# Optimization experiments

Measured on AMD Instinct MI355X. Metric: run time of the kernel, lower is better.

## Reference

```python
import jax, jax.numpy as jnp
import numpy as np

B, N, DIM, H, DH = 4, 2048, 512, 8, 64
INNER = H * DH  # 512
SCALE = DH ** -0.5


def setup_inputs() -> dict:
    key = jax.random.key(0)
    k1, k2, k3, k4 = jax.random.split(key, 4)
    x = jax.random.normal(k1, (B, N, DIM), dtype=jnp.float32)
    bias = jax.random.normal(k2, (B, N, DIM), dtype=jnp.float32)
    # to_qkv: Linear(dim, inner*3, bias=False)
    w_qkv = jax.random.normal(k3, (DIM, 3 * INNER), dtype=jnp.float32) * (DIM ** -0.5)
    # to_out: Linear(inner, dim) with bias (project_out=True since heads != 1)
    w_out = jax.random.normal(k4, (INNER, DIM), dtype=jnp.float32) * (INNER ** -0.5)
    b_out = jnp.zeros((DIM,), dtype=jnp.float32)
    return {"x": x, "bias": bias, "w_qkv": w_qkv, "w_out": w_out, "b_out": b_out}


def _split_heads(t):
    # [b, n, h*d] -> [b, h, n, d]
    b, n, _ = t.shape
    return t.reshape(b, n, H, DH).transpose(0, 2, 1, 3)


def reference(x, bias, w_qkv, w_out, b_out):
    qkv = x @ w_qkv  # [b, n, 3*inner]
    q, k, v = jnp.split(qkv, 3, axis=-1)
    q, k, v = map(_split_heads, (q, k, v))
    dots = jnp.einsum('bhid,bhjd->bhij', q, k) * SCALE  # [b,h,n,n]

    qkv_b = bias @ w_qkv
    qb, kb, _ = jnp.split(qkv_b, 3, axis=-1)
    qb, kb = _split_heads(qb), _split_heads(kb)
    dots = dots + jnp.einsum('bhid,bhjd->bhij', qb, kb) * SCALE

    attn = jax.nn.softmax(dots, axis=-1)
    out = jnp.einsum('bhij,bhjd->bhid', attn, v)  # [b,h,n,d]
    out = out.transpose(0, 2, 1, 3).reshape(x.shape[0], x.shape[1], INNER)
    return out @ w_out + b_out
```

## Files before the change

kernel.cpp:

```cpp
#include <hip/hip_runtime.h>
#include <hip/hip_bf16.h>

#define DEV __device__ __forceinline__

typedef __attribute__((ext_vector_type(8))) short short8;
typedef __attribute__((ext_vector_type(4))) short sv4;
typedef __attribute__((ext_vector_type(4))) float f32x4;

constexpr int B = 4, N = 2048, DIM = 512, H = 8, DH = 64;
constexpr int INNER = H * DH;
constexpr int BH = B * H;
constexpr float SCALE = 0.125f;

constexpr size_t OFF_WQKVT = 0;
constexpr size_t OFF_WOUTT = OFF_WQKVT + (size_t)1536 * 512;
constexpr size_t OFF_QT    = OFF_WOUTT + (size_t)512 * 512;
constexpr size_t OFF_KT    = OFF_QT + (size_t)BH * N * 128;
constexpr size_t OFF_VT    = OFF_KT + (size_t)BH * N * 128;
constexpr size_t OFF_AO    = OFF_VT + (size_t)BH * DH * N;

DEV short f2b(float f) {
    __hip_bfloat16 h = __float2bfloat16(f);
    return __builtin_bit_cast(short, h);
}

DEV void gload16(const void* g, void* l) {
    __builtin_amdgcn_global_load_lds(
        (const __attribute__((address_space(1))) unsigned int*)g,
        (__attribute__((address_space(3))) unsigned int*)l, 16, 0, 0);
}

__global__ void prep_kernel(const float* __restrict__ wqkv,
                            const float* __restrict__ wout,
                            __hip_bfloat16* __restrict__ ws) {
    __hip_bfloat16* wqkvT = ws + OFF_WQKVT;
    __hip_bfloat16* woutT = ws + OFF_WOUTT;
    int tid = blockIdx.x * blockDim.x + threadIdx.x;
    const int total1 = 512 * 1536 / 4;
    const int total2 = 512 * 512 / 4;
    for (int i = tid; i < total1 + total2; i += gridDim.x * blockDim.x) {
        if (i < total1) {
            int k  = i / 384;
            int c4 = (i % 384) * 4;
            float4 v = ((const float4*)wqkv)[i];
            wqkvT[(size_t)(c4 + 0) * 512 + k] = __float2bfloat16(v.x);
            wqkvT[(size_t)(c4 + 1) * 512 + k] = __float2bfloat16(v.y);
            wqkvT[(size_t)(c4 + 2) * 512 + k] = __float2bfloat16(v.z);
            wqkvT[(size_t)(c4 + 3) * 512 + k] = __float2bfloat16(v.w);
        } else {
            int j  = i - total1;
            int k  = j / 128;
            int c4 = (j % 128) * 4;
            float4 v = ((const float4*)wout)[j];
            woutT[(size_t)(c4 + 0) * 512 + k] = __float2bfloat16(v.x);
            woutT[(size_t)(c4 + 1) * 512 + k] = __float2bfloat16(v.y);
            woutT[(size_t)(c4 + 2) * 512 + k] = __float2bfloat16(v.z);
            woutT[(size_t)(c4 + 3) * 512 + k] = __float2bfloat16(v.w);
        }
    }
}

__global__ __launch_bounds__(256) void gemm_qkv(const float* __restrict__ x,
                                                const float* __restrict__ bias,
                                                __hip_bfloat16* __restrict__ ws) {
    int mt = blockIdx.x, yt = blockIdx.y;
    bool src_is_bias = (yt >= 12);
    int nt = src_is_bias ? yt - 12 : yt;
    const float* A = src_is_bias ? bias : x;
    const __hip_bfloat16* Bt = ws + OFF_WQKVT;
    int m0 = mt * 128, n0 = nt * 128;

    __shared__ __align__(16) short As[128][72];
    __shared__ __align__(16) short Bs[128][72];

    int tid  = threadIdx.x;
    int wave = tid >> 6, lane = tid & 63;
    int wrow = wave >> 1, wcol = wave & 1;
    int lg = lane >> 4, li = lane & 15;

    f32x4 acc[4][4] = {};

    for (int k0 = 0; k0 < 512; k0 += 64) {
#pragma unroll
        for (int r = 0; r < 4; ++r) {
            int idx = (tid + r * 256) * 8;
            int row = idx >> 6, kk = idx & 63;
            const float* srcA = A + (size_t)(m0 + row) * 512 + k0 + kk;
            float4 v0 = ((const float4*)srcA)[0];
            float4 v1 = ((const float4*)srcA)[1];
            short8 sv;
            sv[0] = f2b(v0.x); sv[1] = f2b(v0.y); sv[2] = f2b(v0.z); sv[3] = f2b(v0.w);
            sv[4] = f2b(v1.x); sv[5] = f2b(v1.y); sv[6] = f2b(v1.z); sv[7] = f2b(v1.w);
            *(short8*)(&As[row][kk]) = sv;
            const __hip_bfloat16* srcB = Bt + (size_t)(n0 + row) * 512 + k0 + kk;
            *(short8*)(&Bs[row][kk]) = *(const short8*)srcB;
        }
        __syncthreads();
#pragma unroll
        for (int ks = 0; ks < 2; ++ks) {
            short8 af[4], bf[4];
#pragma unroll
            for (int m = 0; m < 4; ++m)
                af[m] = *(const short8*)(&As[wrow * 64 + m * 16 + li][ks * 32 + lg * 8]);
#pragma unroll
            for (int n = 0; n < 4; ++n)
                bf[n] = *(const short8*)(&Bs[wcol * 64 + n * 16 + li][ks * 32 + lg * 8]);
#pragma unroll
            for (int m = 0; m < 4; ++m)
#pragma unroll
                for (int n = 0; n < 4; ++n)
                    acc[m][n] = __builtin_amdgcn_mfma_f32_16x16x32_bf16(af[m], bf[n], acc[m][n], 0, 0, 0);
        }
        __syncthreads();
    }

    __hip_bfloat16* QT = ws + OFF_QT;
    __hip_bfloat16* KT = ws + OFF_KT;
    __hip_bfloat16* VT = ws + OFF_VT;
    int qkoff = src_is_bias ? 64 : 0;
#pragma unroll
    for (int m = 0; m < 4; ++m)
#pragma unroll
        for (int n = 0; n < 4; ++n)
#pragma unroll
            for (int j = 0; j < 4; ++j) {
                int row = m0 + wrow * 64 + m * 16 + lg * 4 + j;
                int col = n0 + wcol * 64 + n * 16 + li;
                float v = acc[m][n][j];
                int b = row >> 11, nn = row & 2047;
                if (col < 512) {
                    int h = col >> 6, d = col & 63;
                    QT[((size_t)(b * H + h) * N + nn) * 128 + d + qkoff] = __float2bfloat16(v * SCALE);
                } else if (col < 1024) {
                    int c = col - 512; int h = c >> 6, d = c & 63;
                    KT[((size_t)(b * H + h) * N + nn) * 128 + d + qkoff] = __float2bfloat16(v);
                } else {
                    int c = col - 1024; int h = c >> 6, d = c & 63;
                    VT[((size_t)(b * H + h) * DH + d) * N + nn] = __float2bfloat16(v);
                }
            }
}

__global__ __launch_bounds__(512, 2) void attn_kernel(__hip_bfloat16* __restrict__ ws) {
    int bid = blockIdx.x;
    int g  = bid >> 6;
    int qb = (bid >> 3) & 7;
    int c  = bid & 7;
    int bh = g * 8 + c;

    int wave = threadIdx.x >> 6, lane = threadIdx.x & 63;
    int lg = lane >> 4, li = lane & 15;
    int qr0 = qb * 256 + wave * 32;

    const short* QT  = (const short*)(ws + OFF_QT) + (size_t)bh * N * 128;
    const char*  KTg = (const char*)((const short*)(ws + OFF_KT) + (size_t)bh * N * 128);
    const char*  VTg = (const char*)((const short*)(ws + OFF_VT) + (size_t)bh * DH * N);

    __shared__ __align__(16) short Ktile[2][64][128];
    __shared__ __align__(16) short Vtile[2][64][64];
    __shared__ __align__(16) short p_lds[8][32][72];

    short8 qf[2][4];
#pragma unroll
    for (int q2 = 0; q2 < 2; ++q2)
#pragma unroll
        for (int kc = 0; kc < 4; ++kc)
            qf[q2][kc] = *(const short8*)(QT + (size_t)(qr0 + q2 * 16 + li) * 128 + kc * 32 + lg * 8);

    float m0 = -3e38f, m1 = -3e38f, l0 = 0.f, l1 = 0.f;
    f32x4 o[2][4] = {};
    char* pbase = (char*)&p_lds[wave][0][0];

    auto stage = [&](int t, int b) {
        int kv0 = t * 64;
#pragma unroll
        for (int cc = 0; cc < 2; ++cc) {
            int ck = wave * 2 + cc;
            int a  = ck * 1024 + lane * 16;
            int r  = a >> 8;
            int cbx = a & 255;
            gload16(KTg + (size_t)(kv0 + r) * 256 + (cbx ^ ((r & 7) << 4)),
                    (char*)&Ktile[b][0][0] + ck * 1024);
        }
        {
            int a  = wave * 1024 + lane * 16;
            int r  = a >> 7;
            int cbx = a & 127;
            gload16(VTg + (size_t)r * 4096 + kv0 * 2 + (cbx ^ ((r & 7) << 4)),
                    (char*)&Vtile[b][0][0] + wave * 1024);
        }
    };

    stage(0, 0);
    __syncthreads();
    int buf = 0;

    for (int t = 0; t < N / 64; ++t) {
        if (t + 1 < N / 64) stage(t + 1, buf ^ 1);
        const char* Kb = (const char*)&Ktile[buf][0][0];
        const char* Vb = (const char*)&Vtile[buf][0][0];

        f32x4 sT[2][4] = {};
#pragma unroll
        for (int cf = 0; cf < 4; ++cf) {
            int rr = cf * 16 + li;
            int sw = (rr & 7) << 4;
#pragma unroll
            for (int kc = 0; kc < 4; ++kc) {
                short8 kf = *(const short8*)(Kb + rr * 256 + ((kc * 64 + lg * 16) ^ sw));
                sT[0][cf] = __builtin_amdgcn_mfma_f32_16x16x32_bf16(kf, qf[0][kc], sT[0][cf], 0, 0, 0);
                sT[1][cf] = __builtin_amdgcn_mfma_f32_16x16x32_bf16(kf, qf[1][kc], sT[1][cf], 0, 0, 0);
            }
        }

        float pm0 = sT[0][0][0], pm1 = sT[1][0][0];
#pragma unroll
        for (int cf = 0; cf < 4; ++cf)
#pragma unroll
            for (int j = 0; j < 4; ++j) {
                pm0 = fmaxf(pm0, sT[0][cf][j]);
                pm1 = fmaxf(pm1, sT[1][cf][j]);
            }
        pm0 = fmaxf(pm0, __shfl_xor(pm0, 16)); pm0 = fmaxf(pm0, __shfl_xor(pm0, 32));
        pm1 = fmaxf(pm1, __shfl_xor(pm1, 16)); pm1 = fmaxf(pm1, __shfl_xor(pm1, 32));

        float a0 = 1.f, a1 = 1.f;
        bool keep = __all((pm0 <= m0 + 8.f) && (pm1 <= m1 + 8.f));
        if (!keep) {
            float mn0 = fmaxf(m0, pm0), mn1 = fmaxf(m1, pm1);
            a0 = __expf(m0 - mn0); a1 = __expf(m1 - mn1);
#pragma unroll
            for (int j = 0; j < 4; ++j) {
                float aj0 = __shfl(a0, lg * 4 + j, 16);
                float aj1 = __shfl(a1, lg * 4 + j, 16);
#pragma unroll
                for (int vc = 0; vc < 4; ++vc) { o[0][vc][j] *= aj0; o[1][vc][j] *= aj1; }
            }
            m0 = mn0; m1 = mn1;
        }

        float ls0 = 0.f, ls1 = 0.f;
#pragma unroll
        for (int cf = 0; cf < 4; ++cf) {
            sv4 w0, w1;
#pragma unroll
            for (int j = 0; j < 4; ++j) {
                float p0 = __expf(sT[0][cf][j] - m0); ls0 += p0; w0[j] = f2b(p0);
                float p1 = __expf(sT[1][cf][j] - m1); ls1 += p1; w1[j] = f2b(p1);
            }
            *(sv4*)(pbase + (size_t)li * 144 + cf * 32 + lg * 8) = w0;
            *(sv4*)(pbase + (size_t)(16 + li) * 144 + cf * 32 + lg * 8) = w1;
        }
        ls0 += __shfl_xor(ls0, 16); ls0 += __shfl_xor(ls0, 32);
        ls1 += __shfl_xor(ls1, 16); ls1 += __shfl_xor(ls1, 32);
        l0 = l0 * a0 + ls0;
        l1 = l1 * a1 + ls1;

        short8 pf0a = *(const short8*)(pbase + (size_t)li * 144 + lg * 16);
        short8 pf0b = *(const short8*)(pbase + (size_t)li * 144 + 64 + lg * 16);
        short8 pf1a = *(const short8*)(pbase + (size_t)(16 + li) * 144 + lg * 16);
        short8 pf1b = *(const short8*)(pbase + (size_t)(16 + li) * 144 + 64 + lg * 16);

#pragma unroll
        for (int vc = 0; vc < 4; ++vc) {
            int dv = vc * 16 + li;
            int sw = (dv & 7) << 4;
            short8 v0 = *(const short8*)(Vb + dv * 128 + ((lg * 16) ^ sw));
            short8 v1 = *(const short8*)(Vb + dv * 128 + ((64 + lg * 16) ^ sw));
            o[0][vc] = __builtin_amdgcn_mfma_f32_16x16x32_bf16(pf0a, v0, o[0][vc], 0, 0, 0);
            o[0][vc] = __builtin_amdgcn_mfma_f32_16x16x32_bf16(pf0b, v1, o[0][vc], 0, 0, 0);
            o[1][vc] = __builtin_amdgcn_mfma_f32_16x16x32_bf16(pf1a, v0, o[1][vc], 0, 0, 0);
            o[1][vc] = __builtin_amdgcn_mfma_f32_16x16x32_bf16(pf1b, v1, o[1][vc], 0, 0, 0);
        }

        __syncthreads();
        buf ^= 1;
    }

    __hip_bfloat16* AO = ws + OFF_AO;
    int b = bh >> 3, h = bh & 7;
#pragma unroll
    for (int q2 = 0; q2 < 2; ++q2) {
        float lq = q2 ? l1 : l0;
#pragma unroll
        for (int j = 0; j < 4; ++j) {
            float lv = __shfl(lq, lg * 4 + j, 16);
            float inv = 1.f / lv;
            int nrow = qr0 + q2 * 16 + lg * 4 + j;
#pragma unroll
            for (int vc = 0; vc < 4; ++vc)
                AO[(size_t)(b * N + nrow) * INNER + h * 64 + vc * 16 + li] =
                    __float2bfloat16(o[q2][vc][j] * inv);
        }
    }
}

__global__ __launch_bounds__(256) void gemm_out(const __hip_bfloat16* __restrict__ ws_c,
                                                const float* __restrict__ bout,
                                                float* __restrict__ out) {
    const __hip_bfloat16* AO = ws_c + OFF_AO;
    const __hip_bfloat16* Bt = ws_c + OFF_WOUTT;
    int m0 = blockIdx.x * 128, n0 = blockIdx.y * 128;

    __shared__ __align__(16) short As[128][72];
    __shared__ __align__(16) short Bs[128][72];

    int tid  = threadIdx.x;
    int wave = tid >> 6, lane = tid & 63;
    int wrow = wave >> 1, wcol = wave & 1;
    int lg = lane >> 4, li = lane & 15;

    f32x4 acc[4][4] = {};

    for (int k0 = 0; k0 < 512; k0 += 64) {
#pragma unroll
        for (int r = 0; r < 4; ++r) {
            int idx = (tid + r * 256) * 8;
            int row = idx >> 6, kk = idx & 63;
            *(short8*)(&As[row][kk]) = *(const short8*)(AO + (size_t)(m0 + row) * 512 + k0 + kk);
            *(short8*)(&Bs[row][kk]) = *(const short8*)(Bt + (size_t)(n0 + row) * 512 + k0 + kk);
        }
        __syncthreads();
#pragma unroll
        for (int ks = 0; ks < 2; ++ks) {
            short8 af[4], bf[4];
#pragma unroll
            for (int m = 0; m < 4; ++m)
                af[m] = *(const short8*)(&As[wrow * 64 + m * 16 + li][ks * 32 + lg * 8]);
#pragma unroll
            for (int n = 0; n < 4; ++n)
                bf[n] = *(const short8*)(&Bs[wcol * 64 + n * 16 + li][ks * 32 + lg * 8]);
#pragma unroll
            for (int m = 0; m < 4; ++m)
#pragma unroll
                for (int n = 0; n < 4; ++n)
                    acc[m][n] = __builtin_amdgcn_mfma_f32_16x16x32_bf16(af[m], bf[n], acc[m][n], 0, 0, 0);
        }
        __syncthreads();
    }
#pragma unroll
    for (int m = 0; m < 4; ++m)
#pragma unroll
        for (int n = 0; n < 4; ++n)
#pragma unroll
            for (int j = 0; j < 4; ++j) {
                int row = m0 + wrow * 64 + m * 16 + lg * 4 + j;
                int col = n0 + wcol * 64 + n * 16 + li;
                out[(size_t)row * 512 + col] = acc[m][n][j] + bout[col];
            }
}

extern "C" void kernel_launch(void* const* d_in, const int* in_sizes, int n_in,
                              void* d_out, int out_size, void* d_ws, size_t ws_size,
                              hipStream_t stream) {
    const float* x    = (const float*)d_in[0];
    const float* bias = (const float*)d_in[1];
    const float* wqkv = (const float*)d_in[2];
    const float* wout = (const float*)d_in[3];
    const float* bout = (const float*)d_in[4];
    float* out = (float*)d_out;
    __hip_bfloat16* ws = (__hip_bfloat16*)d_ws;

    hipLaunchKernelGGL(prep_kernel, dim3(512), dim3(256), 0, stream, wqkv, wout, ws);
    hipLaunchKernelGGL(gemm_qkv, dim3(64, 20), dim3(256), 0, stream, x, bias, ws);
    hipLaunchKernelGGL(attn_kernel, dim3(256), dim3(512), 0, stream, ws);
    hipLaunchKernelGGL(gemm_out, dim3(64, 4), dim3(256), 0, stream, (const __hip_bfloat16*)ws, bout, out);
}
```

Before: 152.6 us.

## Rework attention with 32x32 MFMA, register P, and precast GEMM inputs

The attention kernel moves to 32x32x16 MFMA tiles with 256-thread blocks and a grid of 512. P now stays in registers through permlane32 swaps instead of a round trip through LDS, and a packed bf16 convert plus s_setprio are added. Output goes through LDS so global stores are coalesced. x and bias are cast to bf16 in the prep kernel, and both GEMMs load tiles with direct global-to-LDS loads into unpadded LDS. The precast adds an extra memory pass, and the bias buffer reuses the AO region, which relies on ordering between kernels.

Result: faster. 145.0 us (-5.0%).

```diff
diff --git a/kernel.cpp b/kernel.cpp
--- a/kernel.cpp
+++ b/kernel.cpp
@@ -4,10 +4,12 @@
 #define DEV __device__ __forceinline__
 
 typedef __attribute__((ext_vector_type(8))) short short8;
-typedef __attribute__((ext_vector_type(4))) short sv4;
+typedef __attribute__((ext_vector_type(4))) int i32x4;
+typedef __attribute__((ext_vector_type(2))) int i32x2;
 typedef __attribute__((ext_vector_type(4))) float f32x4;
-
-constexpr int B = 4, N = 2048, DIM = 512, H = 8, DH = 64;
+typedef __attribute__((ext_vector_type(16))) float f32x16;
+
+constexpr int B = 4, N = 2048, H = 8, DH = 64;
 constexpr int INNER = H * DH;
 constexpr int BH = B * H;
 constexpr float SCALE = 0.125f;
@@ -18,10 +20,23 @@
 constexpr size_t OFF_KT    = OFF_QT + (size_t)BH * N * 128;
 constexpr size_t OFF_VT    = OFF_KT + (size_t)BH * N * 128;
 constexpr size_t OFF_AO    = OFF_VT + (size_t)BH * DH * N;
+constexpr size_t OFF_XBF   = OFF_AO + (size_t)8192 * 512;
+constexpr size_t OFF_BBF   = OFF_AO;
 
 DEV short f2b(float f) {
     __hip_bfloat16 h = __float2bfloat16(f);
     return __builtin_bit_cast(short, h);
+}
+
+DEV int cvtpk(float lo, float hi) {
+    int r;
+    asm("v_cvt_pk_bf16_f32 %0, %1, %2" : "=v"(r) : "v"(lo), "v"(hi));
+    return r;
+}
+
+DEV void plswap(int& a, int& b) {
+    i32x2 r = __builtin_amdgcn_permlane32_swap(a, b, false, false);
+    a = r.x; b = r.y;
 }
 
 DEV void gload16(const void* g, void* l) {
@@ -32,23 +47,39 @@
 
 __global__ void prep_kernel(const float* __restrict__ wqkv,
                             const float* __restrict__ wout,
+                            const float* __restrict__ x,
+                            const float* __restrict__ bias,
                             __hip_bfloat16* __restrict__ ws) {
     __hip_bfloat16* wqkvT = ws + OFF_WQKVT;
     __hip_bfloat16* woutT = ws + OFF_WOUTT;
+    short8* xbf = (short8*)(ws + OFF_XBF);
+    short8* bbf = (short8*)(ws + OFF_BBF);
     int tid = blockIdx.x * blockDim.x + threadIdx.x;
-    const int total1 = 512 * 1536 / 4;
-    const int total2 = 512 * 512 / 4;
-    for (int i = tid; i < total1 + total2; i += gridDim.x * blockDim.x) {
-        if (i < total1) {
-            int k  = i / 384;
-            int c4 = (i % 384) * 4;
-            float4 v = ((const float4*)wqkv)[i];
+    const int nconv = 8192 * 512 / 8;
+    const int t1 = 512 * 1536 / 4;
+    const int t2 = 512 * 512 / 4;
+    const int total = 2 * nconv + t1 + t2;
+    for (int i = tid; i < total; i += gridDim.x * blockDim.x) {
+        if (i < 2 * nconv) {
+            const float4* src = (const float4*)(i < nconv ? x : bias);
+            short8* dst = i < nconv ? xbf : bbf;
+            int j = i < nconv ? i : i - nconv;
+            float4 v0 = src[2 * j], v1 = src[2 * j + 1];
+            short8 sv;
+            sv[0] = f2b(v0.x); sv[1] = f2b(v0.y); sv[2] = f2b(v0.z); sv[3] = f2b(v0.w);
+            sv[4] = f2b(v1.x); sv[5] = f2b(v1.y); sv[6] = f2b(v1.z); sv[7] = f2b(v1.w);
+            dst[j] = sv;
+        } else if (i < 2 * nconv + t1) {
+            int j = i - 2 * nconv;
+            int k  = j / 384;
+            int c4 = (j % 384) * 4;
+            float4 v = ((const float4*)wqkv)[j];
             wqkvT[(size_t)(c4 + 0) * 512 + k] = __float2bfloat16(v.x);
             wqkvT[(size_t)(c4 + 1) * 512 + k] = __float2bfloat16(v.y);
             wqkvT[(size_t)(c4 + 2) * 512 + k] = __float2bfloat16(v.z);
             wqkvT[(size_t)(c4 + 3) * 512 + k] = __float2bfloat16(v.w);
         } else {
-            int j  = i - total1;
+            int j = i - 2 * nconv - t1;
             int k  = j / 128;
             int c4 = (j % 128) * 4;
             float4 v = ((const float4*)wout)[j];
@@ -60,18 +91,16 @@
     }
 }
 
-__global__ __launch_bounds__(256) void gemm_qkv(const float* __restrict__ x,
-                                                const float* __restrict__ bias,
-                                                __hip_bfloat16* __restrict__ ws) {
+__global__ __launch_bounds__(256) void gemm_qkv(__hip_bfloat16* __restrict__ ws) {
     int mt = blockIdx.x, yt = blockIdx.y;
     bool src_is_bias = (yt >= 12);
     int nt = src_is_bias ? yt - 12 : yt;
-    const float* A = src_is_bias ? bias : x;
-    const __hip_bfloat16* Bt = ws + OFF_WQKVT;
+    const short* A  = (const short*)(ws + (src_is_bias ? OFF_BBF : OFF_XBF));
+    const short* Bt = (const short*)(ws + OFF_WQKVT);
     int m0 = mt * 128, n0 = nt * 128;
 
-    __shared__ __align__(16) short As[128][72];
-    __shared__ __align__(16) short Bs[128][72];
+    __shared__ __align__(16) short As[128][64];
+    __shared__ __align__(16) short Bs[128][64];
 
     int tid  = threadIdx.x;
     int wave = tid >> 6, lane = tid & 63;
@@ -82,18 +111,13 @@
 
     for (int k0 = 0; k0 < 512; k0 += 64) {
 #pragma unroll
-        for (int r = 0; r < 4; ++r) {
-            int idx = (tid + r * 256) * 8;
-            int row = idx >> 6, kk = idx & 63;
-            const float* srcA = A + (size_t)(m0 + row) * 512 + k0 + kk;
-            float4 v0 = ((const float4*)srcA)[0];
-            float4 v1 = ((const float4*)srcA)[1];
-            short8 sv;
-            sv[0] = f2b(v0.x); sv[1] = f2b(v0.y); sv[2] = f2b(v0.z); sv[3] = f2b(v0.w);
-            sv[4] = f2b(v1.x); sv[5] = f2b(v1.y); sv[6] = f2b(v1.z); sv[7] = f2b(v1.w);
-            *(short8*)(&As[row][kk]) = sv;
-            const __hip_bfloat16* srcB = Bt + (size_t)(n0 + row) * 512 + k0 + kk;
-            *(short8*)(&Bs[row][kk]) = *(const short8*)srcB;
+        for (int i = 0; i < 4; ++i) {
+            int c = wave * 4 + i;
+            int r = c * 8 + (lane >> 3);
+            gload16((const char*)A + ((size_t)(m0 + r) * 512 + k0 + (lane & 7) * 8) * 2,
+                    (char*)&As[0][0] + c * 1024);
+            gload16((const char*)Bt + ((size_t)(n0 + r) * 512 + k0 + (lane & 7) * 8) * 2,
+                    (char*)&Bs[0][0] + c * 1024);
         }
         __syncthreads();
 #pragma unroll
@@ -141,16 +165,16 @@
             }
 }
 
-__global__ __launch_bounds__(512, 2) void attn_kernel(__hip_bfloat16* __restrict__ ws) {
+__global__ __launch_bounds__(256, 3) void attn_kernel(__hip_bfloat16* __restrict__ ws) {
     int bid = blockIdx.x;
-    int g  = bid >> 6;
-    int qb = (bid >> 3) & 7;
-    int c  = bid & 7;
-    int bh = g * 8 + c;
+    int c   = bid & 7;
+    int idx = bid >> 3;
+    int bh  = (idx & 3) * 8 + c;
+    int qb  = idx >> 2;
 
     int wave = threadIdx.x >> 6, lane = threadIdx.x & 63;
-    int lg = lane >> 4, li = lane & 15;
-    int qr0 = qb * 256 + wave * 32;
+    int li32 = lane & 31, hi = lane >> 5;
+    int qr0 = qb * 128 + wave * 32;
 
     const short* QT  = (const short*)(ws + OFF_QT) + (size_t)bh * N * 128;
     const char*  KTg = (const char*)((const short*)(ws + OFF_KT) + (size_t)bh * N * 128);
@@ -158,36 +182,32 @@
 
     __shared__ __align__(16) short Ktile[2][64][128];
     __shared__ __align__(16) short Vtile[2][64][64];
-    __shared__ __align__(16) short p_lds[8][32][72];
-
-    short8 qf[2][4];
-#pragma unroll
-    for (int q2 = 0; q2 < 2; ++q2)
-#pragma unroll
-        for (int kc = 0; kc < 4; ++kc)
-            qf[q2][kc] = *(const short8*)(QT + (size_t)(qr0 + q2 * 16 + li) * 128 + kc * 32 + lg * 8);
-
-    float m0 = -3e38f, m1 = -3e38f, l0 = 0.f, l1 = 0.f;
-    f32x4 o[2][4] = {};
-    char* pbase = (char*)&p_lds[wave][0][0];
+
+    short8 qf[8];
+#pragma unroll
+    for (int kc = 0; kc < 8; ++kc)
+        qf[kc] = *(const short8*)(QT + (size_t)(qr0 + li32) * 128 + kc * 16 + hi * 8);
+
+    float m_run = -3e38f, l_run = 0.f;
+    f32x16 o[2] = {};
 
     auto stage = [&](int t, int b) {
         int kv0 = t * 64;
 #pragma unroll
+        for (int cc = 0; cc < 4; ++cc) {
+            int ck = wave * 4 + cc;
+            int r  = ck * 4 + (lane >> 4);
+            int cbx = (lane & 15) * 16;
+            gload16(KTg + (size_t)(kv0 + r) * 256 + (cbx ^ ((r & 7) << 4)),
+                    (char*)&Ktile[b][0][0] + ck * 1024);
+        }
+#pragma unroll
         for (int cc = 0; cc < 2; ++cc) {
             int ck = wave * 2 + cc;
-            int a  = ck * 1024 + lane * 16;
-            int r  = a >> 8;
-            int cbx = a & 255;
-            gload16(KTg + (size_t)(kv0 + r) * 256 + (cbx ^ ((r & 7) << 4)),
-                    (char*)&Ktile[b][0][0] + ck * 1024);
-        }
-        {
-            int a  = wave * 1024 + lane * 16;
-            int r  = a >> 7;
-            int cbx = a & 127;
+            int r  = ck * 8 + (lane >> 3);
+            int cbx = (lane & 7) * 16;
             gload16(VTg + (size_t)r * 4096 + kv0 * 2 + (cbx ^ ((r & 7) << 4)),
-                    (char*)&Vtile[b][0][0] + wave * 1024);
+                    (char*)&Vtile[b][0][0] + ck * 1024);
         }
     };
 
@@ -200,78 +220,79 @@
         const char* Kb = (const char*)&Ktile[buf][0][0];
         const char* Vb = (const char*)&Vtile[buf][0][0];
 
-        f32x4 sT[2][4] = {};
-#pragma unroll
-        for (int cf = 0; cf < 4; ++cf) {
-            int rr = cf * 16 + li;
-            int sw = (rr & 7) << 4;
-#pragma unroll
-            for (int kc = 0; kc < 4; ++kc) {
-                short8 kf = *(const short8*)(Kb + rr * 256 + ((kc * 64 + lg * 16) ^ sw));
-                sT[0][cf] = __builtin_amdgcn_mfma_f32_16x16x32_bf16(kf, qf[0][kc], sT[0][cf], 0, 0, 0);
-                sT[1][cf] = __builtin_amdgcn_mfma_f32_16x16x32_bf16(kf, qf[1][kc], sT[1][cf], 0, 0, 0);
-            }
-        }
-
-        float pm0 = sT[0][0][0], pm1 = sT[1][0][0];
-#pragma unroll
-        for (int cf = 0; cf < 4; ++cf)
-#pragma unroll
-            for (int j = 0; j < 4; ++j) {
-                pm0 = fmaxf(pm0, sT[0][cf][j]);
-                pm1 = fmaxf(pm1, sT[1][cf][j]);
-            }
-        pm0 = fmaxf(pm0, __shfl_xor(pm0, 16)); pm0 = fmaxf(pm0, __shfl_xor(pm0, 32));
-        pm1 = fmaxf(pm1, __shfl_xor(pm1, 16)); pm1 = fmaxf(pm1, __shfl_xor(pm1, 32));
-
-        float a0 = 1.f, a1 = 1.f;
-        bool keep = __all((pm0 <= m0 + 8.f) && (pm1 <= m1 + 8.f));
-        if (!keep) {
-            float mn0 = fmaxf(m0, pm0), mn1 = fmaxf(m1, pm1);
-            a0 = __expf(m0 - mn0); a1 = __expf(m1 - mn1);
-#pragma unroll
-            for (int j = 0; j < 4; ++j) {
-                float aj0 = __shfl(a0, lg * 4 + j, 16);
-                float aj1 = __shfl(a1, lg * 4 + j, 16);
-#pragma unroll
-                for (int vc = 0; vc < 4; ++vc) { o[0][vc][j] *= aj0; o[1][vc][j] *= aj1; }
-            }
-            m0 = mn0; m1 = mn1;
-        }
-
-        float ls0 = 0.f, ls1 = 0.f;
-#pragma unroll
-        for (int cf = 0; cf < 4; ++cf) {
-            sv4 w0, w1;
-#pragma unroll
-            for (int j = 0; j < 4; ++j) {
-                float p0 = __expf(sT[0][cf][j] - m0); ls0 += p0; w0[j] = f2b(p0);
-                float p1 = __expf(sT[1][cf][j] - m1); ls1 += p1; w1[j] = f2b(p1);
-            }
-            *(sv4*)(pbase + (size_t)li * 144 + cf * 32 + lg * 8) = w0;
-            *(sv4*)(pbase + (size_t)(16 + li) * 144 + cf * 32 + lg * 8) = w1;
-        }
-        ls0 += __shfl_xor(ls0, 16); ls0 += __shfl_xor(ls0, 32);
-        ls1 += __shfl_xor(ls1, 16); ls1 += __shfl_xor(ls1, 32);
-        l0 = l0 * a0 + ls0;
-        l1 = l1 * a1 + ls1;
-
-        short8 pf0a = *(const short8*)(pbase + (size_t)li * 144 + lg * 16);
-        short8 pf0b = *(const short8*)(pbase + (size_t)li * 144 + 64 + lg * 16);
-        short8 pf1a = *(const short8*)(pbase + (size_t)(16 + li) * 144 + lg * 16);
-        short8 pf1b = *(const short8*)(pbase + (size_t)(16 + li) * 144 + 64 + lg * 16);
-
-#pragma unroll
-        for (int vc = 0; vc < 4; ++vc) {
-            int dv = vc * 16 + li;
-            int sw = (dv & 7) << 4;
-            short8 v0 = *(const short8*)(Vb + dv * 128 + ((lg * 16) ^ sw));
-            short8 v1 = *(const short8*)(Vb + dv * 128 + ((64 + lg * 16) ^ sw));
-            o[0][vc] = __builtin_amdgcn_mfma_f32_16x16x32_bf16(pf0a, v0, o[0][vc], 0, 0, 0);
-            o[0][vc] = __builtin_amdgcn_mfma_f32_16x16x32_bf16(pf0b, v1, o[0][vc], 0, 0, 0);
-            o[1][vc] = __builtin_amdgcn_mfma_f32_16x16x32_bf16(pf1a, v0, o[1][vc], 0, 0, 0);
-            o[1][vc] = __builtin_amdgcn_mfma_f32_16x16x32_bf16(pf1b, v1, o[1][vc], 0, 0, 0);
-        }
+        f32x16 sT[2] = {};
+        __builtin_amdgcn_s_setprio(1);
+#pragma unroll
+        for (int sub = 0; sub < 2; ++sub) {
+            int row = sub * 32 + li32;
+            int sw  = (row & 7) << 4;
+            const char* kbase = Kb + row * 256;
+#pragma unroll
+            for (int kc = 0; kc < 8; ++kc) {
+                short8 kf = *(const short8*)(kbase + ((kc * 32 + hi * 16) ^ sw));
+                sT[sub] = __builtin_amdgcn_mfma_f32_32x32x16_bf16(kf, qf[kc], sT[sub], 0, 0, 0);
+            }
+        }
+        __builtin_amdgcn_s_setprio(0);
+
+        float pm = sT[0][0];
+#pragma unroll
+        for (int sub = 0; sub < 2; ++sub)
+#pragma unroll
+            for (int r = 0; r < 16; ++r) pm = fmaxf(pm, sT[sub][r]);
+        pm = fmaxf(pm, __shfl_xor(pm, 32));
+
+        if (__any(pm > m_run + 8.f)) {
+            float mn = fmaxf(m_run, pm);
+            float al = __expf(m_run - mn);
+#pragma unroll
+            for (int a = 0; a < 2; ++a)
+#pragma unroll
+                for (int r = 0; r < 16; ++r) o[a][r] *= al;
+            l_run *= al;
+            m_run = mn;
+        }
+
+        float ls = 0.f;
+        int w[2][8];
+#pragma unroll
+        for (int sub = 0; sub < 2; ++sub)
+#pragma unroll
+            for (int r2 = 0; r2 < 8; ++r2) {
+                float p0 = __expf(sT[sub][2 * r2]     - m_run);
+                float p1 = __expf(sT[sub][2 * r2 + 1] - m_run);
+                ls += p0 + p1;
+                w[sub][r2] = cvtpk(p0, p1);
+            }
+        ls += __shfl_xor(ls, 32);
+        l_run += ls;
+
+        short8 pf[2][2];
+#pragma unroll
+        for (int sub = 0; sub < 2; ++sub) {
+            plswap(w[sub][0], w[sub][2]); plswap(w[sub][1], w[sub][3]);
+            plswap(w[sub][4], w[sub][6]); plswap(w[sub][5], w[sub][7]);
+            i32x4 f0 = { w[sub][0], w[sub][1], w[sub][2], w[sub][3] };
+            i32x4 f1 = { w[sub][4], w[sub][5], w[sub][6], w[sub][7] };
+            pf[sub][0] = __builtin_bit_cast(short8, f0);
+            pf[sub][1] = __builtin_bit_cast(short8, f1);
+        }
+
+        __builtin_amdgcn_s_setprio(1);
+#pragma unroll
+        for (int sub = 0; sub < 2; ++sub)
+#pragma unroll
+            for (int ksel = 0; ksel < 2; ++ksel) {
+                int cc = sub * 2 + ksel;
+#pragma unroll
+                for (int a = 0; a < 2; ++a) {
+                    int row = a * 32 + li32;
+                    int sw  = (row & 7) << 4;
+                    short8 vf = *(const short8*)(Vb + row * 128 + ((cc * 32 + hi * 16) ^ sw));
+                    o[a] = __builtin_amdgcn_mfma_f32_32x32x16_bf16(vf, pf[sub][ksel], o[a], 0, 0, 0);
+                }
+            }
+        __builtin_amdgcn_s_setprio(0);
 
         __syncthreads();
         buf ^= 1;
@@ -279,31 +300,34 @@
 
     __hip_bfloat16* AO = ws + OFF_AO;
     int b = bh >> 3, h = bh & 7;
-#pragma unroll
-    for (int q2 = 0; q2 < 2; ++q2) {
-        float lq = q2 ? l1 : l0;
-#pragma unroll
-        for (int j = 0; j < 4; ++j) {
-            float lv = __shfl(lq, lg * 4 + j, 16);
-            float inv = 1.f / lv;
-            int nrow = qr0 + q2 * 16 + lg * 4 + j;
-#pragma unroll
-            for (int vc = 0; vc < 4; ++vc)
-                AO[(size_t)(b * N + nrow) * INNER + h * 64 + vc * 16 + li] =
-                    __float2bfloat16(o[q2][vc][j] * inv);
-        }
+    char* tb = (char*)&Ktile[0][0][0] + wave * 4096;
+    float inv = 1.f / l_run;
+#pragma unroll
+    for (int a = 0; a < 2; ++a)
+#pragma unroll
+        for (int r2 = 0; r2 < 8; ++r2) {
+            int r = 2 * r2;
+            int dv = (r & 3) + 8 * (r >> 2) + 4 * hi + 32 * a;
+            int word = cvtpk(o[a][r] * inv, o[a][r + 1] * inv);
+            *(int*)(tb + li32 * 128 + ((dv * 2) ^ ((li32 & 7) << 4))) = word;
+        }
+#pragma unroll
+    for (int qq = 0; qq < 32; qq += 8) {
+        int q = qq + (lane >> 3), seg = lane & 7;
+        short8 vrow = *(const short8*)(tb + q * 128 + ((seg * 16) ^ ((q & 7) << 4)));
+        *(short8*)(AO + (size_t)(b * N + qr0 + q) * INNER + h * 64 + seg * 8) = vrow;
     }
 }
 
 __global__ __launch_bounds__(256) void gemm_out(const __hip_bfloat16* __restrict__ ws_c,
                                                 const float* __restrict__ bout,
                                                 float* __restrict__ out) {
-    const __hip_bfloat16* AO = ws_c + OFF_AO;
-    const __hip_bfloat16* Bt = ws_c + OFF_WOUTT;
+    const short* AO = (const short*)(ws_c + OFF_AO);
+    const short* Bt = (const short*)(ws_c + OFF_WOUTT);
     int m0 = blockIdx.x * 128, n0 = blockIdx.y * 128;
 
-    __shared__ __align__(16) short As[128][72];
-    __shared__ __align__(16) short Bs[128][72];
+    __shared__ __align__(16) short As[128][64];
+    __shared__ __align__(16) short Bs[128][64];
 
     int tid  = threadIdx.x;
     int wave = tid >> 6, lane = tid & 63;
@@ -314,11 +338,13 @@
 
     for (int k0 = 0; k0 < 512; k0 += 64) {
 #pragma unroll
-        for (int r = 0; r < 4; ++r) {
-            int idx = (tid + r * 256) * 8;
-            int row = idx >> 6, kk = idx & 63;
-            *(short8*)(&As[row][kk]) = *(const short8*)(AO + (size_t)(m0 + row) * 512 + k0 + kk);
-            *(short8*)(&Bs[row][kk]) = *(const short8*)(Bt + (size_t)(n0 + row) * 512 + k0 + kk);
+        for (int i = 0; i < 4; ++i) {
+            int c = wave * 4 + i;
+            int r = c * 8 + (lane >> 3);
+            gload16((const char*)AO + ((size_t)(m0 + r) * 512 + k0 + (lane & 7) * 8) * 2,
+                    (char*)&As[0][0] + c * 1024);
+            gload16((const char*)Bt + ((size_t)(n0 + r) * 512 + k0 + (lane & 7) * 8) * 2,
+                    (char*)&Bs[0][0] + c * 1024);
         }
         __syncthreads();
 #pragma unroll
@@ -361,8 +387,8 @@
     float* out = (float*)d_out;
     __hip_bfloat16* ws = (__hip_bfloat16*)d_ws;
 
-    hipLaunchKernelGGL(prep_kernel, dim3(512), dim3(256), 0, stream, wqkv, wout, ws);
-    hipLaunchKernelGGL(gemm_qkv, dim3(64, 20), dim3(256), 0, stream, x, bias, ws);
-    hipLaunchKernelGGL(attn_kernel, dim3(256), dim3(512), 0, stream, ws);
+    hipLaunchKernelGGL(prep_kernel, dim3(2048), dim3(256), 0, stream, wqkv, wout, x, bias, ws);
+    hipLaunchKernelGGL(gemm_qkv, dim3(64, 20), dim3(256), 0, stream, ws);
+    hipLaunchKernelGGL(attn_kernel, dim3(512), dim3(256), 0, stream, ws);
     hipLaunchKernelGGL(gemm_out, dim3(64, 4), dim3(256), 0, stream, (const __hip_bfloat16*)ws, bout, out);
 }
```
